# Optimization experiments

Hardware: AMD Instinct MI355X
Metric: run time of the kernel (lower is better)

The kernel has to match this reference:

```python
import jax, jax.numpy as jnp
import numpy as np

B, S, D_IN, D_MID, D_OUT, V = 32, 512, 768, 128, 4, 100000
N = B * S  # static upper bound on number of unique (vocab_id, batch_id) pairs


def setup_inputs() -> dict:
    key = jax.random.key(0)
    k1, k2, k3, k4 = jax.random.split(key, 4)
    vocab_ids = jax.random.randint(k1, (B, S), 0, V)
    embeddings = jax.random.normal(k2, (B, S, D_IN), jnp.float32)
    # nn.Linear default init (kaiming-uniform-ish); exact distribution is irrelevant for correctness
    lin_bound = 1.0 / np.sqrt(D_IN)
    W1 = jax.random.uniform(k3, (D_IN, D_MID), jnp.float32, -lin_bound, lin_bound)
    b1 = jnp.zeros((D_MID,), jnp.float32)
    # kaiming_uniform_(a=sqrt(5)) on (V, D_MID, D_OUT): fan_in = D_MID*D_OUT, bound = 1/sqrt(fan_in)
    enc_bound = 1.0 / np.sqrt(D_MID * D_OUT)
    encoder_weights = jax.random.uniform(k4, (V, D_MID, D_OUT), jnp.float32, -enc_bound, enc_bound)
    return {"vocab_ids": vocab_ids, "embeddings": embeddings, "W1": W1, "b1": b1,
            "encoder_weights": encoder_weights}


def reference(vocab_ids, embeddings, W1, b1, encoder_weights):
    # Composite key = vocab_id * B + batch_id -> same lexicographic (vocab, batch) order
    # as torch.unique(dim=0) on stacked (vocab_id, batch_id) pairs.
    batch_ids = jnp.arange(B, dtype=vocab_ids.dtype)[:, None]            # (B,1)
    keys = (vocab_ids * B + batch_ids).reshape(-1)                        # (N,)
    # Static-size unique for jit; padded slots (fill) receive zero-sum embeddings.
    uniq_keys, inv = jnp.unique(keys, size=N, fill_value=0, return_inverse=True)
    flat_emb = embeddings.reshape(N, D_IN)
    summed = jax.ops.segment_sum(flat_emb, inv.reshape(-1), num_segments=N)  # (N, D_IN)
    h = jnp.tanh(summed @ W1 + b1)                                        # (N, D_MID)
    uniq_vocab = uniq_keys // B
    uniq_batch = uniq_keys % B
    Wtok = encoder_weights[uniq_vocab]                                    # (N, D_MID, D_OUT) gather
    encoded = jax.nn.sigmoid(jnp.einsum('bi,bio->bo', h, Wtok))           # (N, D_OUT)
    ids = jnp.stack([uniq_vocab, uniq_batch], axis=1)                     # (N, 2)
    return ids, encoded
```

## Files before the change

kernel.cpp:

```cpp
#include <hip/hip_runtime.h>
#include <hip/hip_bf16.h>

#define NELEM 16384
#define DIN 768
#define DMID 128
#define DOUT 4

typedef __attribute__((ext_vector_type(8))) short short8;
typedef __attribute__((ext_vector_type(4))) float f32x4;

__device__ __forceinline__ unsigned f2bf(float f) {
    unsigned u = __float_as_uint(f);
    return (u + 0x7FFFu + ((u >> 16) & 1u)) >> 16;
}


#define FAST_WS 557440
#define SB 64

__device__ __forceinline__ unsigned aload(const unsigned* p) {
    return __hip_atomic_load((unsigned*)p, __ATOMIC_RELAXED, __HIP_MEMORY_SCOPE_AGENT);
}
__device__ __forceinline__ void astore(unsigned* p, unsigned v) {
    __hip_atomic_store(p, v, __ATOMIC_RELAXED, __HIP_MEMORY_SCOPE_AGENT);
}
__device__ __forceinline__ void aadd(unsigned* p, unsigned v) {
    __hip_atomic_fetch_add(p, v, __ATOMIC_RELAXED, __HIP_MEMORY_SCOPE_AGENT);
}

__device__ __forceinline__ void gbar(unsigned* cnt, unsigned thresh) {
    __syncthreads();
    if (threadIdx.x == 0) {
        __hip_atomic_fetch_add(cnt, 1u, __ATOMIC_ACQ_REL, __HIP_MEMORY_SCOPE_AGENT);
        while (__hip_atomic_load(cnt, __ATOMIC_RELAXED, __HIP_MEMORY_SCOPE_AGENT) < thresh)
            __builtin_amdgcn_s_sleep(1);
        (void)__hip_atomic_load(cnt, __ATOMIC_ACQUIRE, __HIP_MEMORY_SCOPE_AGENT);
    }
    __syncthreads();
}

template <bool HASNEXT>
__device__ __forceinline__ void scatter_pass(
    const unsigned* __restrict__ src, unsigned* __restrict__ dst,
    const unsigned* __restrict__ histCur, unsigned* __restrict__ histNext,
    int shift, int nshift, int blk, int t,
    unsigned* base_lds, unsigned* whist, unsigned* wsum) {
    const int lane = t & 63;
    const int w = t >> 6;

    unsigned x = aload(&src[blk * 256 + t]);
    unsigned d = (x >> shift) & 255u;

    whist[t] = 0; whist[256 + t] = 0; whist[512 + t] = 0; whist[768 + t] = 0;

    unsigned rowsum = 0, myprefix = 0;
#pragma unroll
    for (int b = 0; b < SB; ++b) {
        unsigned h = aload(&histCur[b * 256 + t]);
        rowsum += h;
        if (b < blk) myprefix += h;
    }
    unsigned inc = rowsum;
#pragma unroll
    for (int off = 1; off < 64; off <<= 1) {
        unsigned y = __shfl_up(inc, off);
        if (lane >= off) inc += y;
    }
    if (lane == 63) wsum[w] = inc;
    __syncthreads();
    unsigned wo = 0;
    for (int w2 = 0; w2 < w; ++w2) wo += wsum[w2];
    base_lds[t] = wo + (inc - rowsum) + myprefix;

    unsigned long long m = ~0ull;
#pragma unroll
    for (int bit = 0; bit < 8; ++bit) {
        unsigned long long bb = __ballot((d >> bit) & 1u);
        m &= ((d >> bit) & 1u) ? bb : ~bb;
    }
    int inrank = __popcll(m & ((1ull << lane) - 1ull));
    if (inrank == 0) whist[w * 256 + d] = (unsigned)__popcll(m);
    __syncthreads();
    unsigned cross = 0;
    for (int w2 = 0; w2 < w; ++w2) cross += whist[w2 * 256 + d];
    unsigned dstpos = base_lds[d] + cross + (unsigned)inrank;
    astore(&dst[dstpos], x);
    if (HASNEXT) {
        unsigned dn = (x >> nshift) & 255u;
        aadd(&histNext[(dstpos >> 8) * 256 + dn], 1u);
    }
    __syncthreads();
}

__global__ __launch_bounds__(256) void sort_mega_kernel(
    const int* __restrict__ vocab_ids, const float* __restrict__ W1,
    unsigned* __restrict__ P0, unsigned* __restrict__ P1,
    unsigned* __restrict__ hist0, unsigned* __restrict__ hist1,
    unsigned* __restrict__ hist2,
    unsigned short* __restrict__ RS, unsigned short* __restrict__ WtG,
    float* __restrict__ out_ids,
    unsigned* __restrict__ bar, unsigned* __restrict__ gsum) {
    __shared__ unsigned base_lds[256];
    __shared__ unsigned whist[4 * 256];
    __shared__ unsigned wsum[4];
    const int t = threadIdx.x;
    const int blk = blockIdx.x;

    const int e = blk * 256 + t;
    {
        whist[t] = 0;
        unsigned word = ((unsigned)vocab_ids[e] << 14) | (unsigned)e;
        astore(&P0[e], word);
        __syncthreads();
        atomicAdd(&whist[(word >> 9) & 255u], 1u);
        __syncthreads();
        astore(&hist0[blk * 256 + t], whist[t]);
        astore(&hist1[blk * 256 + t], 0u);
        astore(&hist2[blk * 256 + t], 0u);
#pragma unroll
        for (int i = 0; i < 6; ++i) {
            int j = blk * 1536 + i * 256 + t;
            int k = j >> 7;
            int c = j & 127;
            WtG[c * DIN + k] = (unsigned short)f2bf(W1[j]);
        }
        __syncthreads();
    }
    gbar(bar, SB * 1);

    scatter_pass<true >(P0, P1, hist0, hist1, 9, 17, blk, t, base_lds, whist, wsum);
    gbar(bar, SB * 2);
    scatter_pass<true >(P1, P0, hist1, hist2, 17, 25, blk, t, base_lds, whist, wsum);
    gbar(bar, SB * 3);
    scatter_pass<false>(P0, P1, hist2, nullptr, 25, 0, blk, t, base_lds, whist, wsum);
    gbar(bar, SB * 4);

    unsigned word = aload(&P1[e]);
    unsigned key = word >> 9;
    bool f = (e == 0) || ((aload(&P1[e - 1]) >> 9) != key);
    {
        const int lane = t & 63;
        const int w = t >> 6;
        unsigned long long bb = __ballot(f ? 1 : 0);
        unsigned lrank = (unsigned)__popcll(bb & ((1ull << lane) - 1ull));
        if (lane == 0) wsum[w] = (unsigned)__popcll(bb);
        __syncthreads();
        unsigned woff = 0, btot = 0;
#pragma unroll
        for (int w2 = 0; w2 < 4; ++w2) {
            if (w2 < w) woff += wsum[w2];
            btot += wsum[w2];
        }
        if (t == 0) astore(&gsum[blk], btot);
        gbar(bar, SB * 5);
        if (t < SB) base_lds[t] = aload(&gsum[t]);
        __syncthreads();
        unsigned prefix = 0, U = 0;
#pragma unroll
        for (int b = 0; b < SB; ++b) {
            unsigned g = base_lds[b];
            if (b < blk) prefix += g;
            U += g;
        }
        if (f) {
            unsigned r = prefix + woff + lrank;
            RS[r] = (unsigned short)e;
            out_ids[2 * r + 0] = (float)(word >> 14);
            out_ids[2 * r + 1] = (float)(key & 31u);
        }
        if ((unsigned)e >= U) {
            RS[e] = (unsigned short)NELEM;
            out_ids[2 * e + 0] = 0.0f;
            out_ids[2 * e + 1] = 0.0f;
        }
        if (e == 0) RS[NELEM] = (unsigned short)NELEM;
    }
}

#define SORT_SMEM (65536 + 65536 + 4096 + 64)

__global__ __launch_bounds__(1024) void sort_transpose_kernel(
    const int* __restrict__ vocab_ids,
    const float* __restrict__ W1,
    unsigned int* __restrict__ G,
    unsigned short* __restrict__ RS,
    unsigned short* __restrict__ WtG,
    float* __restrict__ out_ids) {
    const int t = threadIdx.x;
    if (blockIdx.x != 0) {
        int idx = (blockIdx.x - 1) * 1024 + t;
        if (idx < DMID * DIN) {
            int c = idx / DIN;
            int k = idx - c * DIN;
            WtG[idx] = (unsigned short)f2bf(W1[k * DMID + c]);
        }
        return;
    }
    extern __shared__ char smem[];
    unsigned* Gs     = (unsigned*)smem;
    unsigned* histDM = (unsigned*)(smem + 65536);
    unsigned* sums   = (unsigned*)(smem + 131072);
    unsigned* totalU = (unsigned*)(smem + 135168);

    for (int e = t; e < NELEM; e += 1024)
        Gs[e] = ((unsigned)vocab_ids[e] << 14) | (unsigned)e;
    __syncthreads();

    for (int pass = 0; pass < 6; ++pass) {
        const int shift = 9 + pass * 4;
        unsigned v[16];
#pragma unroll
        for (int i = 0; i < 16; ++i) v[i] = Gs[t * 16 + i];
#pragma unroll
        for (int d = 0; d < 16; ++d) histDM[d * 1024 + t] = 0;
#pragma unroll
        for (int i = 0; i < 16; ++i) histDM[((v[i] >> shift) & 15u) * 1024 + t] += 1;
        __syncthreads();
        unsigned lex[16]; unsigned run = 0;
#pragma unroll
        for (int i = 0; i < 16; ++i) { unsigned x = histDM[t * 16 + i]; lex[i] = run; run += x; }
        sums[t] = run;
        __syncthreads();
        if (t < 64) {
            unsigned s[16]; unsigned tot = 0;
#pragma unroll
            for (int i = 0; i < 16; ++i) { unsigned x = sums[t * 16 + i]; s[i] = tot; tot += x; }
            unsigned incv = tot;
#pragma unroll
            for (int off = 1; off < 64; off <<= 1) {
                unsigned y = __shfl_up(incv, off);
                if (t >= off) incv += y;
            }
            unsigned excl = incv - tot;
#pragma unroll
            for (int i = 0; i < 16; ++i) sums[t * 16 + i] = excl + s[i];
        }
        __syncthreads();
#pragma unroll
        for (int i = 0; i < 16; ++i) histDM[t * 16 + i] = sums[t] + lex[i];
        __syncthreads();
        unsigned mycnt[16];
#pragma unroll
        for (int d = 0; d < 16; ++d) mycnt[d] = histDM[d * 1024 + t];
#pragma unroll
        for (int i = 0; i < 16; ++i) {
            unsigned d = (v[i] >> shift) & 15u;
            Gs[mycnt[d]++] = v[i];
        }
        __syncthreads();
    }

    unsigned v[16];
#pragma unroll
    for (int i = 0; i < 16; ++i) v[i] = Gs[t * 16 + i];
    unsigned pk = (t == 0) ? 0xFFFFFFFFu : (Gs[t * 16 - 1] >> 9);
    unsigned fm = 0;
#pragma unroll
    for (int i = 0; i < 16; ++i) {
        unsigned key = v[i] >> 9;
        if (key != pk) fm |= (1u << i);
        pk = key;
    }
    sums[t] = (unsigned)__popc(fm);
    __syncthreads();
    if (t < 64) {
        unsigned s[16]; unsigned tot = 0;
#pragma unroll
        for (int i = 0; i < 16; ++i) { unsigned x = sums[t * 16 + i]; s[i] = tot; tot += x; }
        unsigned incv = tot;
#pragma unroll
        for (int off = 1; off < 64; off <<= 1) {
            unsigned y = __shfl_up(incv, off);
            if (t >= off) incv += y;
        }
        unsigned excl = incv - tot;
#pragma unroll
        for (int i = 0; i < 16; ++i) sums[t * 16 + i] = excl + s[i];
        if (t == 63) *totalU = incv;
    }
    __syncthreads();
    unsigned r = sums[t];
#pragma unroll
    for (int i = 0; i < 16; ++i) {
        if (fm & (1u << i)) {
            RS[r] = (unsigned short)(t * 16 + i);
            out_ids[2 * r + 0] = (float)(v[i] >> 14);
            out_ids[2 * r + 1] = (float)((v[i] >> 9) & 31u);
            ++r;
        }
    }
    const unsigned U = *totalU;
    for (int u = t; u < NELEM; u += 1024) {
        if ((unsigned)u >= U) {
            RS[u] = (unsigned short)NELEM;
            out_ids[2 * u + 0] = 0.0f;
            out_ids[2 * u + 1] = 0.0f;
        }
        G[u] = Gs[u];
    }
    if (t == 0) RS[NELEM] = (unsigned short)NELEM;
}

#define FBM 16
__global__ __launch_bounds__(256) void fused_kernel(
    const unsigned* __restrict__ G,
    const unsigned short* __restrict__ RS,
    const unsigned short* __restrict__ WtG,
    const float* __restrict__ emb,
    const float* __restrict__ b1,
    const float* __restrict__ enc,
    float* __restrict__ out_enc) {
    __shared__ char smem[20736];

    const int t = threadIdx.x;
    const int u0 = blockIdx.x * FBM;
    const int l = t & 63;
    const int w = t >> 6;

    const int ar = t >> 4;
    const int ak4 = t & 15;
    const int rs_a = (int)RS[u0 + ar];
    const int re_a = (int)RS[u0 + ar + 1];

    f32x4 acc0 = {0.f, 0.f, 0.f, 0.f};
    f32x4 acc1 = {0.f, 0.f, 0.f, 0.f};

    for (int kk = 0; kk < DIN; kk += 64) {
        __syncthreads();
        {
            float s0 = 0.f, s1 = 0.f, s2 = 0.f, s3 = 0.f;
            const float* base = emb + (size_t)(kk + ak4 * 4);
            for (int p = rs_a; p < re_a; ++p) {
                unsigned idx = G[p] & 16383u;
                const float4 e4 = *(const float4*)(base + (size_t)idx * DIN);
                s0 += e4.x; s1 += e4.y; s2 += e4.z; s3 += e4.w;
            }
            uint2 packed;
            packed.x = f2bf(s0) | (f2bf(s1) << 16);
            packed.y = f2bf(s2) | (f2bf(s3) << 16);
            *(uint2*)(smem + ar * 144 + ak4 * 8) = packed;
        }
        {
#pragma unroll
            for (int i = 0; i < 4; ++i) {
                int q = t + i * 256;
                int c = q >> 3;
                int uo = q & 7;
                uint4 dv = *(const uint4*)(WtG + (size_t)c * DIN + kk + uo * 8);
                *(uint4*)(smem + 2304 + c * 144 + uo * 16) = dv;
            }
        }
        __syncthreads();
        {
            const int arow = l & 15;
            const int ull = l >> 4;
#pragma unroll
            for (int kf = 0; kf < 2; ++kf) {
                short8 aF = *(const short8*)(smem + arow * 144 + kf * 64 + ull * 16);
                short8 bF0 = *(const short8*)(smem + 2304 + (w * 32 + arow) * 144 + kf * 64 + ull * 16);
                short8 bF1 = *(const short8*)(smem + 2304 + (w * 32 + 16 + arow) * 144 + kf * 64 + ull * 16);
                acc0 = __builtin_amdgcn_mfma_f32_16x16x32_bf16(aF, bF0, acc0, 0, 0, 0);
                acc1 = __builtin_amdgcn_mfma_f32_16x16x32_bf16(aF, bF1, acc1, 0, 0, 0);
            }
        }
    }
    __syncthreads();
    {
        float* Hs = (float*)smem;
        const int col0 = w * 32 + (l & 15);
        const int rbase = (l >> 4) * 4;
#pragma unroll
        for (int reg = 0; reg < 4; ++reg) {
            Hs[(rbase + reg) * 132 + col0] = tanhf(acc0[reg] + b1[col0]);
            Hs[(rbase + reg) * 132 + col0 + 16] = tanhf(acc1[reg] + b1[col0 + 16]);
        }
    }
    __syncthreads();
    {
        const float* Hs = (const float*)smem;
        const int r = t >> 4;
        const int g = t & 15;
        const int u = u0 + r;
        const int rs = (int)RS[u];
        const int re = (int)RS[u + 1];
        unsigned vocab = (rs < re) ? (G[rs] >> 14) : 0u;
        const float4* wrow = (const float4*)(enc + (size_t)vocab * (DMID * DOUT));
        float ax = 0.f, ay = 0.f, az = 0.f, aw = 0.f;
#pragma unroll
        for (int jj = 0; jj < 8; ++jj) {
            int j = jj * 16 + g;
            float4 w4 = wrow[j];
            float hv = Hs[r * 132 + j];
            ax += hv * w4.x; ay += hv * w4.y; az += hv * w4.z; aw += hv * w4.w;
        }
#pragma unroll
        for (int off = 1; off < 16; off <<= 1) {
            ax += __shfl_xor(ax, off);
            ay += __shfl_xor(ay, off);
            az += __shfl_xor(az, off);
            aw += __shfl_xor(aw, off);
        }
        if (g == 0) {
            float4 o;
            o.x = 1.f / (1.f + expf(-ax));
            o.y = 1.f / (1.f + expf(-ay));
            o.z = 1.f / (1.f + expf(-az));
            o.w = 1.f / (1.f + expf(-aw));
            *(float4*)(out_enc + (size_t)u * 4) = o;
        }
    }
}

extern "C" void kernel_launch(void* const* d_in, const int* in_sizes, int n_in,
                              void* d_out, int out_size, void* d_ws, size_t ws_size,
                              hipStream_t stream) {
    const int*   vocab_ids = (const int*)d_in[0];
    const float* emb       = (const float*)d_in[1];
    const float* W1        = (const float*)d_in[2];
    const float* b1        = (const float*)d_in[3];
    const float* enc       = (const float*)d_in[4];
    float* out = (float*)d_out;

    float* out_ids = out;
    float* out_enc = out + NELEM * 2;

    char* ws = (char*)d_ws;

    if (ws_size >= FAST_WS) {
        unsigned*       P0    = (unsigned*)(ws + 0);
        unsigned*       P1    = (unsigned*)(ws + 65536);
        unsigned*       hist0 = (unsigned*)(ws + 131072);
        unsigned*       hist1 = (unsigned*)(ws + 196608);
        unsigned*       hist2 = (unsigned*)(ws + 262144);
        unsigned short* RS    = (unsigned short*)(ws + 327680);
        unsigned short* WtG   = (unsigned short*)(ws + 360512);
        unsigned*       bar   = (unsigned*)(ws + 557120);
        unsigned*       gsum  = (unsigned*)(ws + 557184);

        hipMemsetAsync(bar, 0, 4, stream);
        sort_mega_kernel<<<SB, 256, 0, stream>>>(vocab_ids, W1, P0, P1,
                                                 hist0, hist1, hist2,
                                                 RS, WtG, out_ids, bar, gsum);
        fused_kernel<<<NELEM / FBM, 256, 0, stream>>>(P1, RS, WtG, emb, b1, enc, out_enc);
    } else {
        unsigned int*   G   = (unsigned int*)(ws);
        unsigned short* RS  = (unsigned short*)(ws + 65536);
        unsigned short* WtG = (unsigned short*)(ws + 98432);

        hipFuncSetAttribute((const void*)sort_transpose_kernel,
                            hipFuncAttributeMaxDynamicSharedMemorySize, SORT_SMEM);
        sort_transpose_kernel<<<1 + 96, 1024, SORT_SMEM, stream>>>(
            vocab_ids, W1, G, RS, WtG, out_ids);
        fused_kernel<<<NELEM / FBM, 256, 0, stream>>>(G, RS, WtG, emb, b1, enc, out_enc);
    }
}
```

Baseline: 66.91 us.

## Replace global radix sort with per-batch bitonic sort and presence bitmap ranking

A new group_kernel replaces the three-pass global radix sort. Each of 32 blocks sorts its own batch's 512 tokens with a shared-memory bitonic sort, while the other 32 blocks set bits in a 100000-word (vocab,batch) presence bitmap. A popcount prefix scan over the bitmap then gives each unique key its output rank. This cuts the number of grid barriers and global scatter passes, but adds a bitmap clear and scan over about 400KB. The fused kernel now reads a packed segment descriptor (batch, start, length) instead of a rank-start array. The new path is used only when the workspace is large enough.

Result: slower. 71.66 us (+7.1%).

```diff
diff --git a/kernel.cpp b/kernel.cpp
--- a/kernel.cpp
+++ b/kernel.cpp
@@ -5,6 +5,7 @@
 #define DIN 768
 #define DMID 128
 #define DOUT 4
+#define NBWORDS 100000
 
 typedef __attribute__((ext_vector_type(8))) short short8;
 typedef __attribute__((ext_vector_type(4))) float f32x4;
@@ -14,18 +15,14 @@
     return (u + 0x7FFFu + ((u >> 16) & 1u)) >> 16;
 }
 
-
-#define FAST_WS 557440
-#define SB 64
-
 __device__ __forceinline__ unsigned aload(const unsigned* p) {
     return __hip_atomic_load((unsigned*)p, __ATOMIC_RELAXED, __HIP_MEMORY_SCOPE_AGENT);
 }
 __device__ __forceinline__ void astore(unsigned* p, unsigned v) {
     __hip_atomic_store(p, v, __ATOMIC_RELAXED, __HIP_MEMORY_SCOPE_AGENT);
 }
-__device__ __forceinline__ void aadd(unsigned* p, unsigned v) {
-    __hip_atomic_fetch_add(p, v, __ATOMIC_RELAXED, __HIP_MEMORY_SCOPE_AGENT);
+__device__ __forceinline__ void aor(unsigned* p, unsigned v) {
+    __hip_atomic_fetch_or(p, v, __ATOMIC_RELAXED, __HIP_MEMORY_SCOPE_AGENT);
 }
 
 __device__ __forceinline__ void gbar(unsigned* cnt, unsigned thresh) {
@@ -37,6 +34,268 @@
         (void)__hip_atomic_load(cnt, __ATOMIC_ACQUIRE, __HIP_MEMORY_SCOPE_AGENT);
     }
     __syncthreads();
+}
+
+#define FAST2_WS 1128000
+
+__global__ __launch_bounds__(256) void group_kernel(
+    const int* __restrict__ vocab_ids, const float* __restrict__ W1,
+    unsigned* __restrict__ Gb, unsigned* __restrict__ bitmap,
+    unsigned* __restrict__ PRE, unsigned* __restrict__ btot,
+    unsigned* __restrict__ SD, unsigned short* __restrict__ WtG,
+    float* __restrict__ out_ids, unsigned* __restrict__ bar) {
+    __shared__ unsigned S[512];
+    __shared__ unsigned red[256];
+    __shared__ unsigned wsumL[4];
+    const int t = threadIdx.x;
+    const int blk = blockIdx.x;
+    const int lane = t & 63;
+    const int wv = t >> 6;
+
+    for (int w = blk * 256 + t; w < NBWORDS; w += 64 * 256) astore(&bitmap[w], 0u);
+#pragma unroll
+    for (int i = 0; i < 6; ++i) {
+        int j = blk * 1536 + i * 256 + t;
+        int k = j >> 7;
+        int c = j & 127;
+        WtG[c * DIN + k] = (unsigned short)f2bf(W1[j]);
+    }
+    gbar(bar, 64);
+
+    if (blk < 32) {
+        const int b = blk;
+        S[t]       = ((unsigned)vocab_ids[b * 512 + t] << 9) | (unsigned)t;
+        S[t + 256] = ((unsigned)vocab_ids[b * 512 + 256 + t] << 9) | (unsigned)(t + 256);
+        const unsigned tu = (unsigned)t;
+        for (unsigned k = 2; k <= 512; k <<= 1) {
+            for (unsigned j = k >> 1; j > 0; j >>= 1) {
+                __syncthreads();
+                unsigned i = ((tu & ~(j - 1)) << 1) | (tu & (j - 1));
+                unsigned p = i | j;
+                bool asc = ((i & k) == 0);
+                unsigned a = S[i], c = S[p];
+                if ((a > c) == asc) { S[i] = c; S[p] = a; }
+            }
+        }
+        __syncthreads();
+        Gb[b * 512 + t] = S[t];
+        Gb[b * 512 + 256 + t] = S[t + 256];
+    } else {
+        const int e0 = (blk - 32) * 512;
+#pragma unroll
+        for (int i = 0; i < 2; ++i) {
+            int e = e0 + i * 256 + t;
+            unsigned key = (unsigned)vocab_ids[e] * 32u + (unsigned)(e >> 9);
+            aor(&bitmap[key >> 5], 1u << (key & 31u));
+        }
+    }
+    gbar(bar, 128);
+
+    const int chunk = blk * 1563;
+    const int lim = (chunk + 1563 < NBWORDS) ? chunk + 1563 : NBWORDS;
+    {
+        unsigned mysum = 0;
+        for (int w = chunk + t; w < lim; w += 256) mysum += (unsigned)__popc(aload(&bitmap[w]));
+        unsigned inc = mysum;
+#pragma unroll
+        for (int off = 1; off < 64; off <<= 1) {
+            unsigned y = __shfl_up(inc, off);
+            if (lane >= off) inc += y;
+        }
+        if (lane == 63) wsumL[wv] = inc;
+        __syncthreads();
+        if (t == 0) astore(&btot[blk], wsumL[0] + wsumL[1] + wsumL[2] + wsumL[3]);
+        __syncthreads();
+    }
+    gbar(bar, 192);
+
+    unsigned U = 0;
+    {
+        if (t < 64) red[t] = aload(&btot[t]);
+        __syncthreads();
+        unsigned base = 0;
+#pragma unroll
+        for (int j = 0; j < 64; ++j) {
+            unsigned g = red[j];
+            if (j < blk) base += g;
+            U += g;
+        }
+        unsigned run = base;
+        for (int r = 0; r < 7; ++r) {
+            int w = chunk + r * 256 + t;
+            unsigned pc = (w < lim) ? (unsigned)__popc(aload(&bitmap[w])) : 0u;
+            unsigned inc = pc;
+#pragma unroll
+            for (int off = 1; off < 64; off <<= 1) {
+                unsigned y = __shfl_up(inc, off);
+                if (lane >= off) inc += y;
+            }
+            if (lane == 63) wsumL[wv] = inc;
+            __syncthreads();
+            unsigned wo = 0, rtot = 0;
+#pragma unroll
+            for (int i = 0; i < 4; ++i) {
+                if (i < wv) wo += wsumL[i];
+                rtot += wsumL[i];
+            }
+            if (w < lim) astore(&PRE[w], run + wo + inc - pc);
+            run += rtot;
+            __syncthreads();
+        }
+    }
+    gbar(bar, 256);
+
+    if (blk < 32) {
+        const int b = blk;
+        S[t] = Gb[b * 512 + t];
+        S[t + 256] = Gb[b * 512 + 256 + t];
+        __syncthreads();
+#pragma unroll
+        for (int q = 0; q < 2; ++q) {
+            int i = q * 256 + t;
+            unsigned wd = S[i];
+            unsigned v = wd >> 9;
+            bool flag = (i == 0) || ((S[i - 1] >> 9) != v);
+            if (flag) {
+                int end = i + 1;
+                while (end < 512 && (S[end] >> 9) == v) ++end;
+                unsigned len = (unsigned)(end - i);
+                unsigned key = v * 32u + (unsigned)b;
+                unsigned bw = key >> 5, bit = key & 31u;
+                unsigned rank = aload(&PRE[bw]) +
+                                (unsigned)__popc(aload(&bitmap[bw]) & ((1u << bit) - 1u));
+                SD[rank] = ((unsigned)b << 19) | ((unsigned)i << 10) | len;
+                out_ids[2 * rank + 0] = (float)v;
+                out_ids[2 * rank + 1] = (float)b;
+            }
+        }
+    } else {
+        for (int u = (int)U + (blk - 32) * 256 + t; u < NELEM; u += 32 * 256) {
+            SD[u] = 0u;
+            out_ids[2 * u + 0] = 0.0f;
+            out_ids[2 * u + 1] = 0.0f;
+        }
+    }
+}
+
+#define FBM 16
+__global__ __launch_bounds__(256) void fused_kernel(
+    const unsigned* __restrict__ Gb,
+    const unsigned* __restrict__ SD,
+    const unsigned short* __restrict__ WtG,
+    const float* __restrict__ emb,
+    const float* __restrict__ b1,
+    const float* __restrict__ enc,
+    float* __restrict__ out_enc) {
+    __shared__ char smem[20736];
+
+    const int t = threadIdx.x;
+    const int u0 = blockIdx.x * FBM;
+    const int l = t & 63;
+    const int w = t >> 6;
+
+    const int ar = t >> 4;
+    const int ak4 = t & 15;
+    const unsigned sdw = SD[u0 + ar];
+    const int lenA = (int)(sdw & 1023u);
+    const unsigned embBase = (sdw >> 19) << 9;
+    const unsigned gb0 = embBase + ((sdw >> 10) & 511u);
+
+    f32x4 acc0 = {0.f, 0.f, 0.f, 0.f};
+    f32x4 acc1 = {0.f, 0.f, 0.f, 0.f};
+
+    for (int kk = 0; kk < DIN; kk += 64) {
+        __syncthreads();
+        {
+            float s0 = 0.f, s1 = 0.f, s2 = 0.f, s3 = 0.f;
+            const float* base = emb + (size_t)(kk + ak4 * 4);
+            for (int p = 0; p < lenA; ++p) {
+                unsigned idx = embBase + (Gb[gb0 + p] & 511u);
+                const float4 e4 = *(const float4*)(base + (size_t)idx * DIN);
+                s0 += e4.x; s1 += e4.y; s2 += e4.z; s3 += e4.w;
+            }
+            uint2 packed;
+            packed.x = f2bf(s0) | (f2bf(s1) << 16);
+            packed.y = f2bf(s2) | (f2bf(s3) << 16);
+            *(uint2*)(smem + ar * 144 + ak4 * 8) = packed;
+        }
+        {
+#pragma unroll
+            for (int i = 0; i < 4; ++i) {
+                int q = t + i * 256;
+                int c = q >> 3;
+                int uo = q & 7;
+                uint4 dv = *(const uint4*)(WtG + (size_t)c * DIN + kk + uo * 8);
+                *(uint4*)(smem + 2304 + c * 144 + uo * 16) = dv;
+            }
+        }
+        __syncthreads();
+        {
+            const int arow = l & 15;
+            const int ull = l >> 4;
+#pragma unroll
+            for (int kf = 0; kf < 2; ++kf) {
+                short8 aF = *(const short8*)(smem + arow * 144 + kf * 64 + ull * 16);
+                short8 bF0 = *(const short8*)(smem + 2304 + (w * 32 + arow) * 144 + kf * 64 + ull * 16);
+                short8 bF1 = *(const short8*)(smem + 2304 + (w * 32 + 16 + arow) * 144 + kf * 64 + ull * 16);
+                acc0 = __builtin_amdgcn_mfma_f32_16x16x32_bf16(aF, bF0, acc0, 0, 0, 0);
+                acc1 = __builtin_amdgcn_mfma_f32_16x16x32_bf16(aF, bF1, acc1, 0, 0, 0);
+            }
+        }
+    }
+    __syncthreads();
+    {
+        float* Hs = (float*)smem;
+        const int col0 = w * 32 + (l & 15);
+        const int rbase = (l >> 4) * 4;
+#pragma unroll
+        for (int reg = 0; reg < 4; ++reg) {
+            Hs[(rbase + reg) * 132 + col0] = tanhf(acc0[reg] + b1[col0]);
+            Hs[(rbase + reg) * 132 + col0 + 16] = tanhf(acc1[reg] + b1[col0 + 16]);
+        }
+    }
+    __syncthreads();
+    {
+        const float* Hs = (const float*)smem;
+        const int r = t >> 4;
+        const int g = t & 15;
+        const int u = u0 + r;
+        const unsigned sdw2 = SD[u];
+        unsigned vocab = 0;
+        if (sdw2 & 1023u)
+            vocab = Gb[((sdw2 >> 19) << 9) + ((sdw2 >> 10) & 511u)] >> 9;
+        const float4* wrow = (const float4*)(enc + (size_t)vocab * (DMID * DOUT));
+        float ax = 0.f, ay = 0.f, az = 0.f, aw = 0.f;
+#pragma unroll
+        for (int jj = 0; jj < 8; ++jj) {
+            int j = jj * 16 + g;
+            float4 w4 = wrow[j];
+            float hv = Hs[r * 132 + j];
+            ax += hv * w4.x; ay += hv * w4.y; az += hv * w4.z; aw += hv * w4.w;
+        }
+#pragma unroll
+        for (int off = 1; off < 16; off <<= 1) {
+            ax += __shfl_xor(ax, off);
+            ay += __shfl_xor(ay, off);
+            az += __shfl_xor(az, off);
+            aw += __shfl_xor(aw, off);
+        }
+        if (g == 0) {
+            float4 o;
+            o.x = 1.f / (1.f + expf(-ax));
+            o.y = 1.f / (1.f + expf(-ay));
+            o.z = 1.f / (1.f + expf(-az));
+            o.w = 1.f / (1.f + expf(-aw));
+            *(float4*)(out_enc + (size_t)u * 4) = o;
+        }
+    }
+}
+
+#define FAST_WS 557440
+#define SB 64
+
+__device__ __forceinline__ void aadd(unsigned* p, unsigned v) {
+    __hip_atomic_fetch_add(p, v, __ATOMIC_RELAXED, __HIP_MEMORY_SCOPE_AGENT);
 }
 
 template <bool HASNEXT>
@@ -47,12 +306,9 @@
     unsigned* base_lds, unsigned* whist, unsigned* wsum) {
     const int lane = t & 63;
     const int w = t >> 6;
-
     unsigned x = aload(&src[blk * 256 + t]);
     unsigned d = (x >> shift) & 255u;
-
     whist[t] = 0; whist[256 + t] = 0; whist[512 + t] = 0; whist[768 + t] = 0;
-
     unsigned rowsum = 0, myprefix = 0;
 #pragma unroll
     for (int b = 0; b < SB; ++b) {
@@ -71,7 +327,6 @@
     unsigned wo = 0;
     for (int w2 = 0; w2 < w; ++w2) wo += wsum[w2];
     base_lds[t] = wo + (inc - rowsum) + myprefix;
-
     unsigned long long m = ~0ull;
 #pragma unroll
     for (int bit = 0; bit < 8; ++bit) {
@@ -105,7 +360,6 @@
     __shared__ unsigned wsum[4];
     const int t = threadIdx.x;
     const int blk = blockIdx.x;
-
     const int e = blk * 256 + t;
     {
         whist[t] = 0;
@@ -127,14 +381,12 @@
         __syncthreads();
     }
     gbar(bar, SB * 1);
-
     scatter_pass<true >(P0, P1, hist0, hist1, 9, 17, blk, t, base_lds, whist, wsum);
     gbar(bar, SB * 2);
     scatter_pass<true >(P1, P0, hist1, hist2, 17, 25, blk, t, base_lds, whist, wsum);
     gbar(bar, SB * 3);
     scatter_pass<false>(P0, P1, hist2, nullptr, 25, 0, blk, t, base_lds, whist, wsum);
     gbar(bar, SB * 4);
-
     unsigned word = aload(&P1[e]);
     unsigned key = word >> 9;
     bool f = (e == 0) || ((aload(&P1[e - 1]) >> 9) != key);
@@ -145,13 +397,13 @@
         unsigned lrank = (unsigned)__popcll(bb & ((1ull << lane) - 1ull));
         if (lane == 0) wsum[w] = (unsigned)__popcll(bb);
         __syncthreads();
-        unsigned woff = 0, btot = 0;
+        unsigned woff = 0, btotv = 0;
 #pragma unroll
         for (int w2 = 0; w2 < 4; ++w2) {
             if (w2 < w) woff += wsum[w2];
-            btot += wsum[w2];
-        }
-        if (t == 0) astore(&gsum[blk], btot);
+            btotv += wsum[w2];
+        }
+        if (t == 0) astore(&gsum[blk], btotv);
         gbar(bar, SB * 5);
         if (t < SB) base_lds[t] = aload(&gsum[t]);
         __syncthreads();
@@ -174,6 +426,111 @@
             out_ids[2 * e + 1] = 0.0f;
         }
         if (e == 0) RS[NELEM] = (unsigned short)NELEM;
+    }
+}
+
+__global__ __launch_bounds__(256) void fused_kernel_rs(
+    const unsigned* __restrict__ G,
+    const unsigned short* __restrict__ RS,
+    const unsigned short* __restrict__ WtG,
+    const float* __restrict__ emb,
+    const float* __restrict__ b1,
+    const float* __restrict__ enc,
+    float* __restrict__ out_enc) {
+    __shared__ char smem[20736];
+    const int t = threadIdx.x;
+    const int u0 = blockIdx.x * FBM;
+    const int l = t & 63;
+    const int w = t >> 6;
+    const int ar = t >> 4;
+    const int ak4 = t & 15;
+    const int rs_a = (int)RS[u0 + ar];
+    const int re_a = (int)RS[u0 + ar + 1];
+    f32x4 acc0 = {0.f, 0.f, 0.f, 0.f};
+    f32x4 acc1 = {0.f, 0.f, 0.f, 0.f};
+    for (int kk = 0; kk < DIN; kk += 64) {
+        __syncthreads();
+        {
+            float s0 = 0.f, s1 = 0.f, s2 = 0.f, s3 = 0.f;
+            const float* base = emb + (size_t)(kk + ak4 * 4);
+            for (int p = rs_a; p < re_a; ++p) {
+                unsigned idx = G[p] & 16383u;
+                const float4 e4 = *(const float4*)(base + (size_t)idx * DIN);
+                s0 += e4.x; s1 += e4.y; s2 += e4.z; s3 += e4.w;
+            }
+            uint2 packed;
+            packed.x = f2bf(s0) | (f2bf(s1) << 16);
+            packed.y = f2bf(s2) | (f2bf(s3) << 16);
+            *(uint2*)(smem + ar * 144 + ak4 * 8) = packed;
+        }
+        {
+#pragma unroll
+            for (int i = 0; i < 4; ++i) {
+                int q = t + i * 256;
+                int c = q >> 3;
+                int uo = q & 7;
+                uint4 dv = *(const uint4*)(WtG + (size_t)c * DIN + kk + uo * 8);
+                *(uint4*)(smem + 2304 + c * 144 + uo * 16) = dv;
+            }
+        }
+        __syncthreads();
+        {
+            const int arow = l & 15;
+            const int ull = l >> 4;
+#pragma unroll
+            for (int kf = 0; kf < 2; ++kf) {
+                short8 aF = *(const short8*)(smem + arow * 144 + kf * 64 + ull * 16);
+                short8 bF0 = *(const short8*)(smem + 2304 + (w * 32 + arow) * 144 + kf * 64 + ull * 16);
+                short8 bF1 = *(const short8*)(smem + 2304 + (w * 32 + 16 + arow) * 144 + kf * 64 + ull * 16);
+                acc0 = __builtin_amdgcn_mfma_f32_16x16x32_bf16(aF, bF0, acc0, 0, 0, 0);
+                acc1 = __builtin_amdgcn_mfma_f32_16x16x32_bf16(aF, bF1, acc1, 0, 0, 0);
+            }
+        }
+    }
+    __syncthreads();
+    {
+        float* Hs = (float*)smem;
+        const int col0 = w * 32 + (l & 15);
+        const int rbase = (l >> 4) * 4;
+#pragma unroll
+        for (int reg = 0; reg < 4; ++reg) {
+            Hs[(rbase + reg) * 132 + col0] = tanhf(acc0[reg] + b1[col0]);
+            Hs[(rbase + reg) * 132 + col0 + 16] = tanhf(acc1[reg] + b1[col0 + 16]);
+        }
+    }
+    __syncthreads();
+    {
+        const float* Hs = (const float*)smem;
+        const int r = t >> 4;
+        const int g = t & 15;
+        const int u = u0 + r;
+        const int rs = (int)RS[u];
+        const int re = (int)RS[u + 1];
+        unsigned vocab = (rs < re) ? (G[rs] >> 14) : 0u;
+        const float4* wrow = (const float4*)(enc + (size_t)vocab * (DMID * DOUT));
+        float ax = 0.f, ay = 0.f, az = 0.f, aw = 0.f;
+#pragma unroll
+        for (int jj = 0; jj < 8; ++jj) {
+            int j = jj * 16 + g;
+            float4 w4 = wrow[j];
+            float hv = Hs[r * 132 + j];
+            ax += hv * w4.x; ay += hv * w4.y; az += hv * w4.z; aw += hv * w4.w;
+        }
+#pragma unroll
+        for (int off = 1; off < 16; off <<= 1) {
+            ax += __shfl_xor(ax, off);
+            ay += __shfl_xor(ay, off);
+            az += __shfl_xor(az, off);
+            aw += __shfl_xor(aw, off);
+        }
+        if (g == 0) {
+            float4 o;
+            o.x = 1.f / (1.f + expf(-ax));
+            o.y = 1.f / (1.f + expf(-ay));
+            o.z = 1.f / (1.f + expf(-az));
+            o.w = 1.f / (1.f + expf(-aw));
+            *(float4*)(out_enc + (size_t)u * 4) = o;
+        }
     }
 }
 
@@ -201,11 +558,9 @@
     unsigned* histDM = (unsigned*)(smem + 65536);
     unsigned* sums   = (unsigned*)(smem + 131072);
     unsigned* totalU = (unsigned*)(smem + 135168);
-
     for (int e = t; e < NELEM; e += 1024)
         Gs[e] = ((unsigned)vocab_ids[e] << 14) | (unsigned)e;
     __syncthreads();
-
     for (int pass = 0; pass < 6; ++pass) {
         const int shift = 9 + pass * 4;
         unsigned v[16];
@@ -249,7 +604,6 @@
         }
         __syncthreads();
     }
-
     unsigned v[16];
 #pragma unroll
     for (int i = 0; i < 16; ++i) v[i] = Gs[t * 16 + i];
@@ -299,116 +653,6 @@
         G[u] = Gs[u];
     }
     if (t == 0) RS[NELEM] = (unsigned short)NELEM;
-}
-
-#define FBM 16
-__global__ __launch_bounds__(256) void fused_kernel(
-    const unsigned* __restrict__ G,
-    const unsigned short* __restrict__ RS,
-    const unsigned short* __restrict__ WtG,
-    const float* __restrict__ emb,
-    const float* __restrict__ b1,
-    const float* __restrict__ enc,
-    float* __restrict__ out_enc) {
-    __shared__ char smem[20736];
-
-    const int t = threadIdx.x;
-    const int u0 = blockIdx.x * FBM;
-    const int l = t & 63;
-    const int w = t >> 6;
-
-    const int ar = t >> 4;
-    const int ak4 = t & 15;
-    const int rs_a = (int)RS[u0 + ar];
-    const int re_a = (int)RS[u0 + ar + 1];
-
-    f32x4 acc0 = {0.f, 0.f, 0.f, 0.f};
-    f32x4 acc1 = {0.f, 0.f, 0.f, 0.f};
-
-    for (int kk = 0; kk < DIN; kk += 64) {
-        __syncthreads();
-        {
-            float s0 = 0.f, s1 = 0.f, s2 = 0.f, s3 = 0.f;
-            const float* base = emb + (size_t)(kk + ak4 * 4);
-            for (int p = rs_a; p < re_a; ++p) {
-                unsigned idx = G[p] & 16383u;
-                const float4 e4 = *(const float4*)(base + (size_t)idx * DIN);
-                s0 += e4.x; s1 += e4.y; s2 += e4.z; s3 += e4.w;
-            }
-            uint2 packed;
-            packed.x = f2bf(s0) | (f2bf(s1) << 16);
-            packed.y = f2bf(s2) | (f2bf(s3) << 16);
-            *(uint2*)(smem + ar * 144 + ak4 * 8) = packed;
-        }
-        {
-#pragma unroll
-            for (int i = 0; i < 4; ++i) {
-                int q = t + i * 256;
-                int c = q >> 3;
-                int uo = q & 7;
-                uint4 dv = *(const uint4*)(WtG + (size_t)c * DIN + kk + uo * 8);
-                *(uint4*)(smem + 2304 + c * 144 + uo * 16) = dv;
-            }
-        }
-        __syncthreads();
-        {
-            const int arow = l & 15;
-            const int ull = l >> 4;
-#pragma unroll
-            for (int kf = 0; kf < 2; ++kf) {
-                short8 aF = *(const short8*)(smem + arow * 144 + kf * 64 + ull * 16);
-                short8 bF0 = *(const short8*)(smem + 2304 + (w * 32 + arow) * 144 + kf * 64 + ull * 16);
-                short8 bF1 = *(const short8*)(smem + 2304 + (w * 32 + 16 + arow) * 144 + kf * 64 + ull * 16);
-                acc0 = __builtin_amdgcn_mfma_f32_16x16x32_bf16(aF, bF0, acc0, 0, 0, 0);
-                acc1 = __builtin_amdgcn_mfma_f32_16x16x32_bf16(aF, bF1, acc1, 0, 0, 0);
-            }
-        }
-    }
-    __syncthreads();
-    {
-        float* Hs = (float*)smem;
-        const int col0 = w * 32 + (l & 15);
-        const int rbase = (l >> 4) * 4;
-#pragma unroll
-        for (int reg = 0; reg < 4; ++reg) {
-            Hs[(rbase + reg) * 132 + col0] = tanhf(acc0[reg] + b1[col0]);
-            Hs[(rbase + reg) * 132 + col0 + 16] = tanhf(acc1[reg] + b1[col0 + 16]);
-        }
-    }
-    __syncthreads();
-    {
-        const float* Hs = (const float*)smem;
-        const int r = t >> 4;
-        const int g = t & 15;
-        const int u = u0 + r;
-        const int rs = (int)RS[u];
-        const int re = (int)RS[u + 1];
-        unsigned vocab = (rs < re) ? (G[rs] >> 14) : 0u;
-        const float4* wrow = (const float4*)(enc + (size_t)vocab * (DMID * DOUT));
-        float ax = 0.f, ay = 0.f, az = 0.f, aw = 0.f;
-#pragma unroll
-        for (int jj = 0; jj < 8; ++jj) {
-            int j = jj * 16 + g;
-            float4 w4 = wrow[j];
-            float hv = Hs[r * 132 + j];
-            ax += hv * w4.x; ay += hv * w4.y; az += hv * w4.z; aw += hv * w4.w;
-        }
-#pragma unroll
-        for (int off = 1; off < 16; off <<= 1) {
-            ax += __shfl_xor(ax, off);
-            ay += __shfl_xor(ay, off);
-            az += __shfl_xor(az, off);
-            aw += __shfl_xor(aw, off);
-        }
-        if (g == 0) {
-            float4 o;
-            o.x = 1.f / (1.f + expf(-ax));
-            o.y = 1.f / (1.f + expf(-ay));
-            o.z = 1.f / (1.f + expf(-az));
-            o.w = 1.f / (1.f + expf(-aw));
-            *(float4*)(out_enc + (size_t)u * 4) = o;
-        }
-    }
 }
 
 extern "C" void kernel_launch(void* const* d_in, const int* in_sizes, int n_in,
@@ -420,13 +664,24 @@
     const float* b1        = (const float*)d_in[3];
     const float* enc       = (const float*)d_in[4];
     float* out = (float*)d_out;
-
     float* out_ids = out;
     float* out_enc = out + NELEM * 2;
-
     char* ws = (char*)d_ws;
 
-    if (ws_size >= FAST_WS) {
+    if (ws_size >= FAST2_WS) {
+        unsigned*       Gb     = (unsigned*)(ws + 0);
+        unsigned*       bitmap = (unsigned*)(ws + 65536);
+        unsigned*       PRE    = (unsigned*)(ws + 465536);
+        unsigned*       btot   = (unsigned*)(ws + 865536);
+        unsigned*       bar    = (unsigned*)(ws + 865792);
+        unsigned*       SD     = (unsigned*)(ws + 865856);
+        unsigned short* WtG    = (unsigned short*)(ws + 931392);
+
+        hipMemsetAsync(bar, 0, 4, stream);
+        group_kernel<<<64, 256, 0, stream>>>(vocab_ids, W1, Gb, bitmap, PRE, btot,
+                                             SD, WtG, out_ids, bar);
+        fused_kernel<<<NELEM / FBM, 256, 0, stream>>>(Gb, SD, WtG, emb, b1, enc, out_enc);
+    } else if (ws_size >= FAST_WS) {
         unsigned*       P0    = (unsigned*)(ws + 0);
         unsigned*       P1    = (unsigned*)(ws + 65536);
         unsigned*       hist0 = (unsigned*)(ws + 131072);
@@ -441,7 +696,7 @@
         sort_mega_kernel<<<SB, 256, 0, stream>>>(vocab_ids, W1, P0, P1,
                                                  hist0, hist1, hist2,
                                                  RS, WtG, out_ids, bar, gsum);
-        fused_kernel<<<NELEM / FBM, 256, 0, stream>>>(P1, RS, WtG, emb, b1, enc, out_enc);
+        fused_kernel_rs<<<NELEM / FBM, 256, 0, stream>>>(P1, RS, WtG, emb, b1, enc, out_enc);
     } else {
         unsigned int*   G   = (unsigned int*)(ws);
         unsigned short* RS  = (unsigned short*)(ws + 65536);
@@ -451,6 +706,6 @@
                             hipFuncAttributeMaxDynamicSharedMemorySize, SORT_SMEM);
         sort_transpose_kernel<<<1 + 96, 1024, SORT_SMEM, stream>>>(
             vocab_ids, W1, G, RS, WtG, out_ids);
-        fused_kernel<<<NELEM / FBM, 256, 0, stream>>>(G, RS, WtG, emb, b1, enc, out_enc);
-    }
-}
+        fused_kernel_rs<<<NELEM / FBM, 256, 0, stream>>>(G, RS, WtG, emb, b1, enc, out_enc);
+    }
+}
```
